# Kernel optimization log

Hardware: AMD Instinct MI355X
Metric: run time of the kernel (lower is better)

Reference implementation:

```python
import jax, jax.numpy as jnp
import numpy as np

HIDDEN = 128
VEL_SCALE = 0.5
T_END = 1.0


def conv1x1(x, w, b):
    # x: [B, Cin, N], w: [Cout, Cin], b: [Cout]
    return jnp.einsum('oi,bin->bon', w, x) + b[None, :, None]


def setup_inputs() -> dict:
    key = jax.random.key(0)
    ks = jax.random.split(key, 11)
    B, N = 8, 50000
    def winit(k, shape, fan_in):
        bound = 1.0 / np.sqrt(fan_in)
        return jax.random.uniform(k, shape, jnp.float32, -bound, bound)
    return {
        'x0': jax.random.normal(ks[0], (B, 3, N), jnp.float32),
        'h1_w': winit(ks[1], (HIDDEN, 4), 4), 'h1_b': winit(ks[2], (HIDDEN,), 4),
        'g1_w': winit(ks[3], (HIDDEN, 4), 4), 'g1_b': winit(ks[4], (HIDDEN,), 4),
        'h2_w': winit(ks[5], (HIDDEN, HIDDEN), HIDDEN), 'h2_b': winit(ks[6], (HIDDEN,), HIDDEN),
        'g2_w': winit(ks[7], (HIDDEN, HIDDEN), HIDDEN), 'g2_b': winit(ks[8], (HIDDEN,), HIDDEN),
        'out_w': winit(ks[9], (3, HIDDEN), HIDDEN), 'out_b': winit(ks[10], (3,), HIDDEN),
    }


def field(t, x, h1_w, h1_b, g1_w, g1_b, h2_w, h2_b, g2_w, g2_b, out_w, out_b):
    B, _, N = x.shape
    t_chan = jnp.broadcast_to(jnp.reshape(t, (1, 1, 1)), (B, 1, N))
    z = jnp.concatenate([x, t_chan], axis=1)                 # [B, 4, N]
    z = conv1x1(z, h1_w, h1_b) * jax.nn.sigmoid(conv1x1(z, g1_w, g1_b))
    z = jax.nn.relu(z)
    z = conv1x1(z, h2_w, h2_b) * jax.nn.sigmoid(conv1x1(z, g2_w, g2_b))
    z = jax.nn.relu(z)
    v = conv1x1(z, out_w, out_b)                             # [B, 3, N]
    return jnp.tanh(v) * VEL_SCALE


def reference(x0, h1_w, h1_b, g1_w, g1_b, h2_w, h2_b, g2_w, g2_b, out_w, out_b):
    params = (h1_w, h1_b, g1_w, g1_b, h2_w, h2_b, g2_w, g2_b, out_w, out_b)
    f = lambda t, y: field(jnp.asarray(t, jnp.float32), y, *params)
    # torchdiffeq 'rk4' with t=[0, T] and no step_size: single 3/8-rule RK4 step, h = T
    h = jnp.float32(T_END)
    t0 = jnp.float32(0.0)
    third = jnp.float32(1.0 / 3.0)
    k1 = f(t0, x0)
    k2 = f(t0 + h * third, x0 + h * k1 * third)
    k3 = f(t0 + h * third * 2.0, x0 + h * (k2 - k1 * third))
    k4 = f(t0 + h, x0 + h * (k1 - k2 + k3))
    return x0 + h * (k1 + 3.0 * (k2 + k3) + k4) * jnp.float32(0.125)
```

## Files before the change

### kernel.cpp

```cpp
#include <hip/hip_runtime.h>
#include <math.h>
#include <utility>

typedef __attribute__((ext_vector_type(8))) short    bf16x8;
typedef __attribute__((ext_vector_type(4))) float    f32x4;
typedef __attribute__((ext_vector_type(2))) float    f32x2;
typedef __attribute__((ext_vector_type(2))) unsigned u32x2;
typedef __attribute__((ext_vector_type(4))) unsigned u32x4;

template<int I, int N, class F>
__device__ __forceinline__ void sfor(F&& f) {
    if constexpr (I < N) { f(std::integral_constant<int, I>{}); sfor<I + 1, N>(static_cast<F&&>(f)); }
}

#define NPT    50000
#define NBLK   3125
#define Z_S    128
#define LOG2E  1.4426950408889634f

#define OFF_Z1   0
#define OFF_Z2   32768
#define OFF_ZIN  65536
#define OFF_KST  67584
#define OFF_AOW  73728
#define OFF_BIAS 74496
#define OFF_A1   76608
#define LDS_BYTES 78656
#define TBZ   8192
#define TBZIN 512
#define TBK   768

static __device__ __forceinline__ unsigned short bf16r(float f) {
    unsigned u = __builtin_bit_cast(unsigned, f);
    u += 0x7FFFu + ((u >> 16) & 1u);
    return (unsigned short)(u >> 16);
}

#if defined(__has_builtin)
#if __has_builtin(__builtin_amdgcn_cvt_pk_bf16_f32)
#define HAVE_CVT_PK_BF16 1
#endif
#if __has_builtin(__builtin_amdgcn_exp2f) && __has_builtin(__builtin_amdgcn_rcpf)
#define HAVE_RAW_TRANS 1
#endif
#endif

static __device__ __forceinline__ unsigned packbf(float a, float b) {
#ifdef HAVE_CVT_PK_BF16
    return __builtin_bit_cast(unsigned, __builtin_amdgcn_cvt_pk_bf16_f32(a, b));
#else
    return (unsigned)bf16r(a) | ((unsigned)bf16r(b) << 16);
#endif
}

#ifdef HAVE_RAW_TRANS
static __device__ __forceinline__ float fexp2(float x) { return __builtin_amdgcn_exp2f(x); }
static __device__ __forceinline__ float frcp(float x)  { return __builtin_amdgcn_rcpf(x); }
#else
static __device__ __forceinline__ float fexp2(float x) { return __exp2f(x); }
static __device__ __forceinline__ float frcp(float x)  { return __frcp_rn(x); }
#endif

static __device__ __forceinline__ unsigned gate2p(f32x2 h, f32x2 gp) {
    f32x2 e;
    e.x = fexp2(gp.x);
    e.y = fexp2(gp.y);
    f32x2 p = e + 1.f;
    float ip = frcp(p.x * p.y);
    f32x2 ps = __builtin_shufflevector(p, p, 1, 0);
    f32x2 z = (h * ps) * ip;
    z = __builtin_elementwise_max(z, f32x2{0.f, 0.f});
    return packbf(z.x, z.y);
}

static __device__ __forceinline__ bf16x8 pack8s(const float* p, float s) {
    f32x4 lo = *reinterpret_cast<const f32x4*>(p);
    f32x4 hi = *reinterpret_cast<const f32x4*>(p + 4);
    u32x4 u = { packbf(lo[0]*s, lo[1]*s), packbf(lo[2]*s, lo[3]*s),
                packbf(hi[0]*s, hi[1]*s), packbf(hi[2]*s, hi[3]*s) };
    return __builtin_bit_cast(bf16x8, u);
}
static __device__ __forceinline__ f32x4 mfma16(bf16x8 a, bf16x8 b, f32x4 c) {
    return __builtin_amdgcn_mfma_f32_16x16x32_bf16(a, b, c, 0, 0, 0);
}

__global__ __launch_bounds__(512, 4) void node_rk4_mfma(
    const float* __restrict__ x0,
    const float* __restrict__ h1_w, const float* __restrict__ h1_b,
    const float* __restrict__ g1_w, const float* __restrict__ g1_b,
    const float* __restrict__ h2_w, const float* __restrict__ h2_b,
    const float* __restrict__ g2_w, const float* __restrict__ g2_b,
    const float* __restrict__ out_w, const float* __restrict__ out_b,
    float* __restrict__ y)
{
    extern __shared__ char lds_raw[];
    short*    z1s    = reinterpret_cast<short*>(lds_raw + OFF_Z1);
    short*    z2s    = reinterpret_cast<short*>(lds_raw + OFF_Z2);
    short*    zin    = reinterpret_cast<short*>(lds_raw + OFF_ZIN);
    float*    kst    = reinterpret_cast<float*>(lds_raw + OFF_KST);
    short*    aow_s  = reinterpret_cast<short*>(lds_raw + OFF_AOW);
    float*    bias_s = reinterpret_cast<float*>(lds_raw + OFF_BIAS);
    unsigned* a1_s   = reinterpret_cast<unsigned*>(lds_raw + OFF_A1);

    const int tid  = threadIdx.x;
    const int w    = tid >> 6;
    const int lane = tid & 63;
    const int q    = lane >> 4;
    const int m    = lane & 15;

    const int row = 16 * w + m;
    bf16x8 a2h[4], a2g[4];
    sfor<0, 4>([&](auto KS) {
        constexpr int ks = KS.value;
        a2h[ks] = pack8s(h2_w + row * 128 + ks * 32 + q * 8, 1.0f);
        a2g[ks] = pack8s(g2_w + row * 128 + ks * 32 + q * 8, -LOG2E);
    });
    if (tid < 128) {
        const f32x4 t1 = *reinterpret_cast<const f32x4*>(h1_w + tid * 4);
        const f32x4 t2 = *reinterpret_cast<const f32x4*>(g1_w + tid * 4);
        a1_s[tid * 2]           = packbf(t1[0], t1[1]);
        a1_s[tid * 2 + 1]       = packbf(t1[2], t1[3]);
        a1_s[256 + tid * 2]     = packbf(t2[0] * -LOG2E, t2[1] * -LOG2E);
        a1_s[256 + tid * 2 + 1] = packbf(t2[2] * -LOG2E, t2[3] * -LOG2E);
    }
    if (w == 0 && m < 3) {
        sfor<0, 4>([&](auto KS) {
            constexpr int ks = KS.value;
            bf16x8 t = pack8s(out_w + m * 128 + ks * 32 + q * 8, 2.f * LOG2E);
            *reinterpret_cast<bf16x8*>(&aow_s[((ks * 3 + m) * 4 + q) * 8]) = t;
        });
    }
    if (tid < 128) {
        bias_s[tid]       = h1_b[tid];
        bias_s[128 + tid] = g1_b[tid] * -LOG2E;
        bias_s[256 + tid] = h2_b[tid];
        bias_s[384 + tid] = g2_b[tid] * -LOG2E;
    }
    if (tid < 16) bias_s[512 + tid] = (tid < 3) ? out_b[tid] * (2.f * LOG2E) : 0.f;

    if (tid < 128) *reinterpret_cast<u32x4*>(&zin[tid * 8]) = u32x4{0u, 0u, 0u, 0u};
    __syncthreads();

    const float third = 1.0f / 3.0f;
    const int cb4 = 16 * w + 4 * q;

    const int m7   = m & 7;
    const int qx8  = (q ^ (m & 3)) * 8;
    const int m4_8 = (m & 4) * 8;

    const short* zin_rd = &zin[m * 8];
    short*       zin_wr = &zin[row * 8];
    const short* z1_re  = &z1s[m * Z_S + qx8 + m4_8];
    const short* z1_ro  = &z1s[m * Z_S + qx8 + (m4_8 ^ 32)];
    short*       z1_wr  = &z1s[m * Z_S + (((2 * w + (q >> 1)) ^ m7) * 8) + (q & 1) * 4];
    short*       z2_wr  = &z2s[m * Z_S + (((2 * w + (q >> 1)) ^ m7) * 8) + (q & 1) * 4];
    const short* z2_re  = &z2s[(16 * w + m) * Z_S + qx8 + m4_8];
    const short* z2_ro  = &z2s[(16 * w + m) * Z_S + qx8 + (m4_8 ^ 32)];
    const short* aow_rd = &aow_s[((m < 3 ? m : 2) * 4 + q) * 8];
    const float* bs     = &bias_s[cb4];
    const float* bsov   = &bias_s[512 + 4 * q];
    float*       kbase  = &kst[row * 4];

    float xcA0=0.f, xcA1=0.f, xcA2=0.f, xcB0=0.f, xcB1=0.f, xcB2=0.f;
    int gbA = 0, gbB = 0;
    if (w < 4 && lane < 16) {
        const int pgA = blockIdx.x * 128 + row;
        const int bbA = pgA / NPT;
        gbA = bbA * 3 * NPT + (pgA - bbA * NPT);
        xcA0 = x0[gbA]; xcA1 = x0[gbA + NPT]; xcA2 = x0[gbA + 2 * NPT];
        const int pgB = pgA + 64;
        const int bbB = pgB / NPT;
        gbB = bbB * 3 * NPT + (pgB - bbB * NPT);
        xcB0 = x0[gbB]; xcB1 = x0[gbB + NPT]; xcB2 = x0[gbB + 2 * NPT];
    }
    float axA=0.f, ayA=0.f, azA=0.f, axB=0.f, ayB=0.f, azB=0.f;

    #pragma unroll 1
    for (int s = 0; s < 4; ++s) {
        if (w < 4 && lane < 16) {
            auto STAGET = [&](auto TT, float x0c, float x1c, float x2c) {
                constexpr int T = TT.value;
                const float* kb = kbase + T * TBK;
                float zi0, zi1, zi2, tt;
                if (s == 0)      { zi0 = x0c; zi1 = x1c; zi2 = x2c; tt = 0.f; }
                else if (s == 1) {
                    f32x4 k1 = *reinterpret_cast<const f32x4*>(kb);
                    zi0 = fmaf(k1[0], third, x0c);
                    zi1 = fmaf(k1[1], third, x1c);
                    zi2 = fmaf(k1[2], third, x2c); tt = third;
                } else if (s == 2) {
                    f32x4 k1 = *reinterpret_cast<const f32x4*>(kb);
                    f32x4 k2 = *reinterpret_cast<const f32x4*>(kb + 256);
                    zi0 = x0c + (k2[0] - k1[0] * third);
                    zi1 = x1c + (k2[1] - k1[1] * third);
                    zi2 = x2c + (k2[2] - k1[2] * third); tt = 2.f * third;
                } else {
                    f32x4 k1 = *reinterpret_cast<const f32x4*>(kb);
                    f32x4 k2 = *reinterpret_cast<const f32x4*>(kb + 256);
                    f32x4 k3 = *reinterpret_cast<const f32x4*>(kb + 512);
                    zi0 = x0c + (k1[0] - k2[0] + k3[0]);
                    zi1 = x1c + (k1[1] - k2[1] + k3[1]);
                    zi2 = x2c + (k1[2] - k2[2] + k3[2]); tt = 1.f;
                }
                u32x2 pk = { packbf(zi0, zi1), packbf(zi2, tt) };
                *reinterpret_cast<u32x2*>(zin_wr + T * TBZIN) = pk;
            };
            STAGET(std::integral_constant<int, 0>{}, xcA0, xcA1, xcA2);
            STAGET(std::integral_constant<int, 1>{}, xcB0, xcB1, xcB2);
        }
        __syncthreads();

        {
            bf16x8 a1h = {0,0,0,0,0,0,0,0}, a1g = {0,0,0,0,0,0,0,0};
            if (q == 0) {
                u32x2 th = *reinterpret_cast<const u32x2*>(&a1_s[row * 2]);
                u32x2 tg = *reinterpret_cast<const u32x2*>(&a1_s[256 + row * 2]);
                u32x4 uh = { th[0], th[1], 0u, 0u };
                u32x4 ug = { tg[0], tg[1], 0u, 0u };
                a1h = __builtin_bit_cast(bf16x8, uh);
                a1g = __builtin_bit_cast(bf16x8, ug);
            }
            const f32x4 b1h = *reinterpret_cast<const f32x4*>(bs);
            const f32x4 b1g = *reinterpret_cast<const f32x4*>(bs + 128);
            auto L1T = [&](auto TT) {
                constexpr int T = TT.value;
                sfor<0, 4>([&](auto NT) {
                    constexpr int nt = NT.value;
                    bf16x8 bf = *reinterpret_cast<const bf16x8*>(zin_rd + T * TBZIN + nt * 128);
                    f32x4 ch = mfma16(a1h, bf, b1h);
                    f32x4 cg = mfma16(a1g, bf, b1g);
                    u32x2 pk = { gate2p(f32x2{ch[0], ch[1]}, f32x2{cg[0], cg[1]}),
                                 gate2p(f32x2{ch[2], ch[3]}, f32x2{cg[2], cg[3]}) };
                    *reinterpret_cast<u32x2*>(z1_wr + T * TBZ + nt * 2048) = pk;
                });
            };
            L1T(std::integral_constant<int, 0>{});
            L1T(std::integral_constant<int, 1>{});
        }
        __syncthreads();

        {
            const f32x4 b2h = *reinterpret_cast<const f32x4*>(bs + 256);
            const f32x4 b2g = *reinterpret_cast<const f32x4*>(bs + 384);
            auto L2T = [&](auto TT) {
                constexpr int T = TT.value;
                sfor<0, 2>([&](auto NTP) {
                    constexpr int b0 = T * TBZ + (2 * NTP.value) * 2048;
                    constexpr int b1 = T * TBZ + (2 * NTP.value + 1) * 2048;
                    f32x4 c0h, c1h, c0g, c1g;
                    {
                        bf16x8 f0 = *reinterpret_cast<const bf16x8*>(z1_re + b0);
                        bf16x8 f1 = *reinterpret_cast<const bf16x8*>(z1_re + b1);
                        c0h = mfma16(a2h[0], f0, b2h); c1h = mfma16(a2h[0], f1, b2h);
                        c0g = mfma16(a2g[0], f0, b2g); c1g = mfma16(a2g[0], f1, b2g);
                    }
                    sfor<1, 4>([&](auto KS) {
                        constexpr int ks = KS.value;
                        const short* zb = (ks & 1) ? z1_ro : z1_re;
                        constexpr int koff = (ks & 2) ? 64 : 0;
                        bf16x8 f0 = *reinterpret_cast<const bf16x8*>(zb + b0 + koff);
                        bf16x8 f1 = *reinterpret_cast<const bf16x8*>(zb + b1 + koff);
                        c0h = mfma16(a2h[ks], f0, c0h); c1h = mfma16(a2h[ks], f1, c1h);
                        c0g = mfma16(a2g[ks], f0, c0g); c1g = mfma16(a2g[ks], f1, c1g);
                    });
                    u32x2 pk0 = { gate2p(f32x2{c0h[0], c0h[1]}, f32x2{c0g[0], c0g[1]}),
                                  gate2p(f32x2{c0h[2], c0h[3]}, f32x2{c0g[2], c0g[3]}) };
                    *reinterpret_cast<u32x2*>(z2_wr + b0) = pk0;
                    u32x2 pk1 = { gate2p(f32x2{c1h[0], c1h[1]}, f32x2{c1g[0], c1g[1]}),
                                  gate2p(f32x2{c1h[2], c1h[3]}, f32x2{c1g[2], c1g[3]}) };
                    *reinterpret_cast<u32x2*>(z2_wr + b1) = pk1;
                });
            };
            L2T(std::integral_constant<int, 0>{});
            L2T(std::integral_constant<int, 1>{});
        }
        __syncthreads();

        if (w < 4) {
            auto OUTT = [&](auto TT, float& ax, float& ay, float& az) {
                constexpr int T = TT.value;
                f32x4 vc = *reinterpret_cast<const f32x4*>(bsov);
                sfor<0, 4>([&](auto KS) {
                    constexpr int ks = KS.value;
                    bf16x8 af = *reinterpret_cast<const bf16x8*>(aow_rd + ks * 96);
                    const short* zb = (ks & 1) ? z2_ro : z2_re;
                    constexpr int koff = (ks & 2) ? 64 : 0;
                    bf16x8 bf = *reinterpret_cast<const bf16x8*>(zb + T * TBZ + koff);
                    vc = mfma16(af, bf, vc);
                });
                f32x2 e; e.x = fexp2(vc[0]); e.y = fexp2(vc[1]);
                f32x2 p = e + 1.f;
                const float ipxy = frcp(p.x * p.y);
                const float kx = 0.5f - p.y * ipxy;
                const float ky = 0.5f - p.x * ipxy;
                const float kz = 0.5f - frcp(fexp2(vc[2]) + 1.f);
                if (lane < 16 && s < 3)
                    *reinterpret_cast<f32x4*>(kbase + T * TBK + s * 256) = f32x4{kx, ky, kz, 0.f};
                if (s == 0)      { ax = kx; ay = ky; az = kz; }
                else if (s < 3)  { ax = fmaf(3.f, kx, ax); ay = fmaf(3.f, ky, ay); az = fmaf(3.f, kz, az); }
                else             { ax += kx; ay += ky; az += kz; }
            };
            OUTT(std::integral_constant<int, 0>{}, axA, ayA, azA);
            OUTT(std::integral_constant<int, 1>{}, axB, ayB, azB);
        }
    }

    if (w < 4 && lane < 16) {
        y[gbA]           = fmaf(0.125f, axA, xcA0);
        y[gbA + NPT]     = fmaf(0.125f, ayA, xcA1);
        y[gbA + 2 * NPT] = fmaf(0.125f, azA, xcA2);
        y[gbB]           = fmaf(0.125f, axB, xcB0);
        y[gbB + NPT]     = fmaf(0.125f, ayB, xcB1);
        y[gbB + 2 * NPT] = fmaf(0.125f, azB, xcB2);
    }
}

extern "C" void kernel_launch(void* const* d_in, const int* in_sizes, int n_in,
                              void* d_out, int out_size, void* d_ws, size_t ws_size,
                              hipStream_t stream) {
    (void)in_sizes; (void)n_in; (void)d_ws; (void)ws_size; (void)out_size;
    const float* x0    = (const float*)d_in[0];
    const float* h1_w  = (const float*)d_in[1];
    const float* h1_b  = (const float*)d_in[2];
    const float* g1_w  = (const float*)d_in[3];
    const float* g1_b  = (const float*)d_in[4];
    const float* h2_w  = (const float*)d_in[5];
    const float* h2_b  = (const float*)d_in[6];
    const float* g2_w  = (const float*)d_in[7];
    const float* g2_b  = (const float*)d_in[8];
    const float* out_w = (const float*)d_in[9];
    const float* out_b = (const float*)d_in[10];
    float* y = (float*)d_out;

    static bool attr_set = false;
    if (!attr_set) {
        (void)hipFuncSetAttribute(reinterpret_cast<const void*>(&node_rk4_mfma),
                                  hipFuncAttributeMaxDynamicSharedMemorySize, LDS_BYTES);
        attr_set = true;
    }
    node_rk4_mfma<<<NBLK, 512, LDS_BYTES, stream>>>(
        x0, h1_w, h1_b, g1_w, g1_b, h2_w, h2_b, g2_w, g2_b, out_w, out_b, y);
}
```

Baseline: 279.4 us.

## Fuse RK stage staging into output epilogue and spread output work across all waves

```diff
diff --git a/kernel.cpp b/kernel.cpp
--- a/kernel.cpp
+++ b/kernel.cpp
@@ -22,13 +22,12 @@
 #define OFF_Z2   32768
 #define OFF_ZIN  65536
 #define OFF_KST  67584
-#define OFF_AOW  73728
-#define OFF_BIAS 74496
-#define OFF_A1   76608
-#define LDS_BYTES 78656
+#define OFF_AOW  71680
+#define OFF_BIAS 72448
+#define OFF_A1   74560
+#define LDS_BYTES 76608
 #define TBZ   8192
 #define TBZIN 512
-#define TBK   768
 
 static __device__ __forceinline__ unsigned short bf16r(float f) {
     unsigned u = __builtin_bit_cast(unsigned, f);
@@ -139,7 +138,6 @@
     if (tid < 16) bias_s[512 + tid] = (tid < 3) ? out_b[tid] * (2.f * LOG2E) : 0.f;
 
     if (tid < 128) *reinterpret_cast<u32x4*>(&zin[tid * 8]) = u32x4{0u, 0u, 0u, 0u};
-    __syncthreads();
 
     const float third = 1.0f / 3.0f;
     const int cb4 = 16 * w + 4 * q;
@@ -154,62 +152,31 @@
     const short* z1_ro  = &z1s[m * Z_S + qx8 + (m4_8 ^ 32)];
     short*       z1_wr  = &z1s[m * Z_S + (((2 * w + (q >> 1)) ^ m7) * 8) + (q & 1) * 4];
     short*       z2_wr  = &z2s[m * Z_S + (((2 * w + (q >> 1)) ^ m7) * 8) + (q & 1) * 4];
-    const short* z2_re  = &z2s[(16 * w + m) * Z_S + qx8 + m4_8];
-    const short* z2_ro  = &z2s[(16 * w + m) * Z_S + qx8 + (m4_8 ^ 32)];
+    const short* z2_re  = &z2s[row * Z_S + qx8 + m4_8];
+    const short* z2_ro  = &z2s[row * Z_S + qx8 + (m4_8 ^ 32)];
     const short* aow_rd = &aow_s[((m < 3 ? m : 2) * 4 + q) * 8];
     const float* bs     = &bias_s[cb4];
     const float* bsov   = &bias_s[512 + 4 * q];
     float*       kbase  = &kst[row * 4];
 
-    float xcA0=0.f, xcA1=0.f, xcA2=0.f, xcB0=0.f, xcB1=0.f, xcB2=0.f;
-    int gbA = 0, gbB = 0;
-    if (w < 4 && lane < 16) {
-        const int pgA = blockIdx.x * 128 + row;
-        const int bbA = pgA / NPT;
-        gbA = bbA * 3 * NPT + (pgA - bbA * NPT);
-        xcA0 = x0[gbA]; xcA1 = x0[gbA + NPT]; xcA2 = x0[gbA + 2 * NPT];
-        const int pgB = pgA + 64;
-        const int bbB = pgB / NPT;
-        gbB = bbB * 3 * NPT + (pgB - bbB * NPT);
-        xcB0 = x0[gbB]; xcB1 = x0[gbB + NPT]; xcB2 = x0[gbB + 2 * NPT];
-    }
-    float axA=0.f, ayA=0.f, azA=0.f, axB=0.f, ayB=0.f, azB=0.f;
+    float xc0 = 0.f, xc1 = 0.f, xc2 = 0.f;
+    int gbase = 0;
+    if (lane < 16) {
+        const int pg = blockIdx.x * 128 + row;
+        const int bb = pg / NPT;
+        gbase = bb * 3 * NPT + (pg - bb * NPT);
+        xc0 = x0[gbase]; xc1 = x0[gbase + NPT]; xc2 = x0[gbase + 2 * NPT];
+    }
+    float ax = 0.f, ay = 0.f, az = 0.f;
+
+    if (lane < 16) {
+        u32x2 pk = { packbf(xc0, xc1), packbf(xc2, 0.f) };
+        *reinterpret_cast<u32x2*>(zin_wr) = pk;
+    }
+    __syncthreads();
 
     #pragma unroll 1
     for (int s = 0; s < 4; ++s) {
-        if (w < 4 && lane < 16) {
-            auto STAGET = [&](auto TT, float x0c, float x1c, float x2c) {
-                constexpr int T = TT.value;
-                const float* kb = kbase + T * TBK;
-                float zi0, zi1, zi2, tt;
-                if (s == 0)      { zi0 = x0c; zi1 = x1c; zi2 = x2c; tt = 0.f; }
-                else if (s == 1) {
-                    f32x4 k1 = *reinterpret_cast<const f32x4*>(kb);
-                    zi0 = fmaf(k1[0], third, x0c);
-                    zi1 = fmaf(k1[1], third, x1c);
-                    zi2 = fmaf(k1[2], third, x2c); tt = third;
-                } else if (s == 2) {
-                    f32x4 k1 = *reinterpret_cast<const f32x4*>(kb);
-                    f32x4 k2 = *reinterpret_cast<const f32x4*>(kb + 256);
-                    zi0 = x0c + (k2[0] - k1[0] * third);
-                    zi1 = x1c + (k2[1] - k1[1] * third);
-                    zi2 = x2c + (k2[2] - k1[2] * third); tt = 2.f * third;
-                } else {
-                    f32x4 k1 = *reinterpret_cast<const f32x4*>(kb);
-                    f32x4 k2 = *reinterpret_cast<const f32x4*>(kb + 256);
-                    f32x4 k3 = *reinterpret_cast<const f32x4*>(kb + 512);
-                    zi0 = x0c + (k1[0] - k2[0] + k3[0]);
-                    zi1 = x1c + (k1[1] - k2[1] + k3[1]);
-                    zi2 = x2c + (k1[2] - k2[2] + k3[2]); tt = 1.f;
-                }
-                u32x2 pk = { packbf(zi0, zi1), packbf(zi2, tt) };
-                *reinterpret_cast<u32x2*>(zin_wr + T * TBZIN) = pk;
-            };
-            STAGET(std::integral_constant<int, 0>{}, xcA0, xcA1, xcA2);
-            STAGET(std::integral_constant<int, 1>{}, xcB0, xcB1, xcB2);
-        }
-        __syncthreads();
-
         {
             bf16x8 a1h = {0,0,0,0,0,0,0,0}, a1g = {0,0,0,0,0,0,0,0};
             if (q == 0) {
@@ -222,7 +189,7 @@
             }
             const f32x4 b1h = *reinterpret_cast<const f32x4*>(bs);
             const f32x4 b1g = *reinterpret_cast<const f32x4*>(bs + 128);
-            auto L1T = [&](auto TT) {
+            sfor<0, 2>([&](auto TT) {
                 constexpr int T = TT.value;
                 sfor<0, 4>([&](auto NT) {
                     constexpr int nt = NT.value;
@@ -233,16 +200,14 @@
                                  gate2p(f32x2{ch[2], ch[3]}, f32x2{cg[2], cg[3]}) };
                     *reinterpret_cast<u32x2*>(z1_wr + T * TBZ + nt * 2048) = pk;
                 });
-            };
-            L1T(std::integral_constant<int, 0>{});
-            L1T(std::integral_constant<int, 1>{});
+            });
         }
         __syncthreads();
 
         {
             const f32x4 b2h = *reinterpret_cast<const f32x4*>(bs + 256);
             const f32x4 b2g = *reinterpret_cast<const f32x4*>(bs + 384);
-            auto L2T = [&](auto TT) {
+            sfor<0, 2>([&](auto TT) {
                 constexpr int T = TT.value;
                 sfor<0, 2>([&](auto NTP) {
                     constexpr int b0 = T * TBZ + (2 * NTP.value) * 2048;
@@ -270,48 +235,67 @@
                                   gate2p(f32x2{c1h[2], c1h[3]}, f32x2{c1g[2], c1g[3]}) };
                     *reinterpret_cast<u32x2*>(z2_wr + b1) = pk1;
                 });
-            };
-            L2T(std::integral_constant<int, 0>{});
-            L2T(std::integral_constant<int, 1>{});
+            });
         }
         __syncthreads();
 
-        if (w < 4) {
-            auto OUTT = [&](auto TT, float& ax, float& ay, float& az) {
-                constexpr int T = TT.value;
-                f32x4 vc = *reinterpret_cast<const f32x4*>(bsov);
-                sfor<0, 4>([&](auto KS) {
-                    constexpr int ks = KS.value;
-                    bf16x8 af = *reinterpret_cast<const bf16x8*>(aow_rd + ks * 96);
-                    const short* zb = (ks & 1) ? z2_ro : z2_re;
-                    constexpr int koff = (ks & 2) ? 64 : 0;
-                    bf16x8 bf = *reinterpret_cast<const bf16x8*>(zb + T * TBZ + koff);
-                    vc = mfma16(af, bf, vc);
-                });
-                f32x2 e; e.x = fexp2(vc[0]); e.y = fexp2(vc[1]);
-                f32x2 p = e + 1.f;
-                const float ipxy = frcp(p.x * p.y);
-                const float kx = 0.5f - p.y * ipxy;
-                const float ky = 0.5f - p.x * ipxy;
-                const float kz = 0.5f - frcp(fexp2(vc[2]) + 1.f);
-                if (lane < 16 && s < 3)
-                    *reinterpret_cast<f32x4*>(kbase + T * TBK + s * 256) = f32x4{kx, ky, kz, 0.f};
-                if (s == 0)      { ax = kx; ay = ky; az = kz; }
-                else if (s < 3)  { ax = fmaf(3.f, kx, ax); ay = fmaf(3.f, ky, ay); az = fmaf(3.f, kz, az); }
-                else             { ax += kx; ay += ky; az += kz; }
-            };
-            OUTT(std::integral_constant<int, 0>{}, axA, ayA, azA);
-            OUTT(std::integral_constant<int, 1>{}, axB, ayB, azB);
+        {
+            f32x4 vc = *reinterpret_cast<const f32x4*>(bsov);
+            sfor<0, 4>([&](auto KS) {
+                constexpr int ks = KS.value;
+                bf16x8 af = *reinterpret_cast<const bf16x8*>(aow_rd + ks * 96);
+                const short* zb = (ks & 1) ? z2_ro : z2_re;
+                constexpr int koff = (ks & 2) ? 64 : 0;
+                bf16x8 bf = *reinterpret_cast<const bf16x8*>(zb + koff);
+                vc = mfma16(af, bf, vc);
+            });
+            f32x2 e; e.x = fexp2(vc[0]); e.y = fexp2(vc[1]);
+            f32x2 p = e + 1.f;
+            const float ipxy = frcp(p.x * p.y);
+            const float kx = 0.5f - p.y * ipxy;
+            const float ky = 0.5f - p.x * ipxy;
+            const float kz = 0.5f - frcp(fexp2(vc[2]) + 1.f);
+
+            if (lane < 16) {
+                float zi0, zi1, zi2, tt;
+                bool do_stage = true;
+                if (s == 0) {
+                    ax = kx; ay = ky; az = kz;
+                    *reinterpret_cast<f32x4*>(kbase) = f32x4{kx, ky, kz, 0.f};
+                    zi0 = fmaf(kx, third, xc0);
+                    zi1 = fmaf(ky, third, xc1);
+                    zi2 = fmaf(kz, third, xc2); tt = third;
+                } else if (s == 1) {
+                    ax = fmaf(3.f, kx, ax); ay = fmaf(3.f, ky, ay); az = fmaf(3.f, kz, az);
+                    f32x4 k1 = *reinterpret_cast<const f32x4*>(kbase);
+                    *reinterpret_cast<f32x4*>(kbase + 512) = f32x4{kx, ky, kz, 0.f};
+                    zi0 = xc0 + (kx - k1[0] * third);
+                    zi1 = xc1 + (ky - k1[1] * third);
+                    zi2 = xc2 + (kz - k1[2] * third); tt = 2.f * third;
+                } else if (s == 2) {
+                    ax = fmaf(3.f, kx, ax); ay = fmaf(3.f, ky, ay); az = fmaf(3.f, kz, az);
+                    f32x4 k1 = *reinterpret_cast<const f32x4*>(kbase);
+                    f32x4 k2 = *reinterpret_cast<const f32x4*>(kbase + 512);
+                    zi0 = xc0 + (k1[0] - k2[0] + kx);
+                    zi1 = xc1 + (k1[1] - k2[1] + ky);
+                    zi2 = xc2 + (k1[2] - k2[2] + kz); tt = 1.f;
+                } else {
+                    ax += kx; ay += ky; az += kz;
+                    do_stage = false; zi0 = zi1 = zi2 = tt = 0.f;
+                }
+                if (do_stage) {
+                    u32x2 pk = { packbf(zi0, zi1), packbf(zi2, tt) };
+                    *reinterpret_cast<u32x2*>(zin_wr) = pk;
+                }
+            }
         }
-    }
-
-    if (w < 4 && lane < 16) {
-        y[gbA]           = fmaf(0.125f, axA, xcA0);
-        y[gbA + NPT]     = fmaf(0.125f, ayA, xcA1);
-        y[gbA + 2 * NPT] = fmaf(0.125f, azA, xcA2);
-        y[gbB]           = fmaf(0.125f, axB, xcB0);
-        y[gbB + NPT]     = fmaf(0.125f, ayB, xcB1);
-        y[gbB + 2 * NPT] = fmaf(0.125f, azB, xcB2);
+        if (s < 3) __syncthreads();
+    }
+
+    if (lane < 16) {
+        y[gbase]           = fmaf(0.125f, ax, xc0);
+        y[gbase + NPT]     = fmaf(0.125f, ay, xc1);
+        y[gbase + 2 * NPT] = fmaf(0.125f, az, xc2);
     }
 }
 
```

After: 270.8 us. -3.1%, faster.
